# Performance work log

Measured on AMD Instinct MI355X. Metric: run time of the kernel, lower is better.

The kernel has to match this reference:

```python
import jax, jax.numpy as jnp
import numpy as np

B, S, D, H = 4, 1024, 256, 8  # batch, seq, d_model (== head_dim), n_heads
SCALE = 1.0 / float(np.sqrt(D))  # source references undefined self.scale; use 1/sqrt(d_model)


def setup_inputs() -> dict:
    key = jax.random.key(0)
    ks = jax.random.split(key, 11)
    w = 0.02
    return {
        "value_input": jax.random.normal(ks[0], (B, S, D), dtype=jnp.float32),
        "key_input": jax.random.normal(ks[1], (B, S, D), dtype=jnp.float32),
        "query_input": jax.random.normal(ks[2], (B, S, D), dtype=jnp.float32),
        "Wv": jax.random.normal(ks[3], (D, D * H), dtype=jnp.float32) * w,
        "bv": jnp.zeros((D * H,), dtype=jnp.float32),
        "Wk": jax.random.normal(ks[4], (D, D * H), dtype=jnp.float32) * w,
        "bk": jnp.zeros((D * H,), dtype=jnp.float32),
        "Wq": jax.random.normal(ks[5], (D, D * H), dtype=jnp.float32) * w,
        "bq": jnp.zeros((D * H,), dtype=jnp.float32),
        "Wo": jax.random.normal(ks[6], (D * H, D), dtype=jnp.float32) * w,
        "bo": jnp.zeros((D,), dtype=jnp.float32),
    }


def reference(value_input, key_input, query_input, Wv, bv, Wk, bk, Wq, bq, Wo, bo):
    # Fused QKV-style projections, then split into heads along last dim.
    # torch.split(..., d_model, dim=-1) == reshape to (B, S, H, D).
    v = (value_input @ Wv + bv).reshape(B, S, H, D)
    k = (key_input @ Wk + bk).reshape(B, S, H, D)
    q = (query_input @ Wq + bq).reshape(B, S, H, D)
    # Source: dot = k @ q^T  -> scores[b,h,key_pos,query_pos]
    scores = jnp.einsum('bkhd,bqhd->bhkq', k, q) * SCALE
    # Softmax over dim=-1 == the QUERY axis (faithful to source, nonstandard).
    attn = jax.nn.softmax(scores, axis=-1)
    # attn @ v : contract query axis with v's seq axis -> output indexed by key pos
    out_h = jnp.einsum('bhkq,bqhd->bkhd', attn, v)
    concat = out_h.reshape(B, S, H * D)
    return concat @ Wo + bo
```

## Files before the change

### kernel.cpp

```cpp
#include <hip/hip_runtime.h>
#include <cstddef>
#include <cstdint>

#define Bz 4
#define Sz 1024
#define Dm 256
#define Hh 8
#define DHh 2048
#define SCALE 0.0625f

typedef __attribute__((ext_vector_type(8))) short short8;
typedef __attribute__((ext_vector_type(16))) float f32x16;

__device__ inline unsigned short f2bf(float f){
  unsigned u = __float_as_uint(f);
  u += 0x7FFFu + ((u >> 16) & 1u);
  return (unsigned short)(u >> 16);
}
__device__ inline unsigned pk2(float a, float b){
  return (unsigned)f2bf(a) | ((unsigned)f2bf(b) << 16);
}
__device__ inline void gll16(const void* g, void* l){
  __builtin_amdgcn_global_load_lds((const __attribute__((address_space(1))) unsigned*)g,
                                   (__attribute__((address_space(3))) unsigned*)l, 16, 0, 0);
}
__device__ inline short8 lds8(const char* p){ return *(const short8*)p; }
__device__ inline f32x16 MM(short8 a, short8 b, f32x16 c){
  return __builtin_amdgcn_mfma_f32_32x32x16_bf16(a, b, c, 0, 0, 0);
}
__device__ inline f32x16 z16(){ f32x16 v;
#pragma unroll
  for(int i=0;i<16;i++) v[i]=0.f; return v; }

__global__ __launch_bounds__(256) void cvt_a(
    const float* __restrict__ S0, const float* __restrict__ S1, const float* __restrict__ S2,
    unsigned short* __restrict__ D0, unsigned short* __restrict__ D1, unsigned short* __restrict__ D2){
  const int bx = blockIdx.x;
  const int seg = bx >> 10;
  const float* src = seg==0 ? S0 : seg==1 ? S1 : S2;
  unsigned short* dst = seg==0 ? D0 : seg==1 ? D1 : D2;
  const int i = (bx & 1023)*256 + threadIdx.x;
  float4 v = ((const float4*)src)[i];
  ushort4 o; o.x=f2bf(v.x); o.y=f2bf(v.y); o.z=f2bf(v.z); o.w=f2bf(v.w);
  ((ushort4*)dst)[i] = o;
}

__global__ __launch_bounds__(256) void cvt_w(
    const float* __restrict__ W0, const float* __restrict__ W1,
    const float* __restrict__ W2, const float* __restrict__ W3,
    unsigned short* __restrict__ T0, unsigned short* __restrict__ T1,
    unsigned short* __restrict__ T2, unsigned short* __restrict__ T3){
  __shared__ float t[32][33];
  const int z = blockIdx.z;
  const float* W = z==0 ? W0 : z==1 ? W1 : z==2 ? W2 : W3;
  unsigned short* T = z==0 ? T0 : z==1 ? T1 : z==2 ? T2 : T3;
  const int K = (z<3) ? 256 : 2048;
  const int N = (z<3) ? 2048 : 256;
  const int n0 = (z<3) ? blockIdx.x*32 : blockIdx.y*32;
  const int k0 = (z<3) ? blockIdx.y*32 : blockIdx.x*32;
  const int a = threadIdx.x >> 5, c = threadIdx.x & 31;
#pragma unroll
  for(int p=0;p<4;p++)
    t[a + p*8][c] = W[(size_t)(k0 + a + p*8)*N + n0 + c];
  __syncthreads();
#pragma unroll
  for(int p=0;p<4;p++)
    T[(size_t)(n0 + a + p*8)*K + k0 + c] = f2bf(t[c][a + p*8]);
}

template<int VAR>
__global__ __launch_bounds__(256) void gemm_proj(const unsigned short* __restrict__ A,
    const unsigned short* __restrict__ Bt, const float* __restrict__ bias,
    unsigned short* __restrict__ C){
  __shared__ __align__(16) char sm[65536];
  const int tid = threadIdx.x, w = tid>>6, lane = tid&63, l31 = lane&31, hp = lane>>5;
  const int wm = (w>>1)*64, wn = (w&1)*64;
  const int bm = blockIdx.y*128, bn = blockIdx.x*128;
  f32x16 acc[2][2]; acc[0][0]=z16(); acc[0][1]=z16(); acc[1][0]=z16(); acc[1][1]=z16();

  auto STAGE = [&](int db, int kk){
#pragma unroll
    for(int j=0;j<4;j++){
      int ci = (w*4+j)*64 + lane;
      int m = ci>>3, sl = ci&7;
      gll16(A  + (size_t)(bm+m)*256 + kk + ((sl ^ (m&7))<<3), sm + db*32768 + (w*4+j)*1024);
      gll16(Bt + (size_t)(bn+m)*256 + kk + ((sl ^ (m&7))<<3), sm + db*32768 + 16384 + (w*4+j)*1024);
    }
  };

  STAGE(0, 0);
  __syncthreads();
  int db = 0;
  for(int t=0; t<4; ++t){
    if(t<3) STAGE(db^1, (t+1)*64);
    const char* base = sm + db*32768;
#pragma unroll
    for(int s=0;s<4;s++){
      int m0 = wm + l31, m1 = wm + 32 + l31;
      int n0 = wn + l31, n1 = wn + 32 + l31;
      short8 a0 = lds8(base + m0*128 + (((s*2+hp) ^ (m0&7))<<4));
      short8 a1 = lds8(base + m1*128 + (((s*2+hp) ^ (m1&7))<<4));
      short8 b0 = lds8(base + 16384 + n0*128 + (((s*2+hp) ^ (n0&7))<<4));
      short8 b1 = lds8(base + 16384 + n1*128 + (((s*2+hp) ^ (n1&7))<<4));
      acc[0][0] = MM(a0,b0,acc[0][0]); acc[0][1] = MM(a0,b1,acc[0][1]);
      acc[1][0] = MM(a1,b0,acc[1][0]); acc[1][1] = MM(a1,b1,acc[1][1]);
    }
    __syncthreads();
    db ^= 1;
  }
#pragma unroll
  for(int nh=0; nh<2; nh++){
    int ncol = bn + wn + nh*32 + l31;
    float bb = bias[ncol];
#pragma unroll
    for(int mh=0; mh<2; mh++){
      if(VAR == 2){
        int hidx = ncol >> 8, d = ncol & 255;
#pragma unroll
        for(int g=0; g<4; g++){
          int mrow = bm + wm + mh*32 + 8*g + 4*hp;
          int batch = mrow >> 10, sin = mrow & 1023;
          unsigned u0 = pk2(acc[mh][nh][4*g+0] + bb, acc[mh][nh][4*g+1] + bb);
          unsigned u1 = pk2(acc[mh][nh][4*g+2] + bb, acc[mh][nh][4*g+3] + bb);
          uint2 uu; uu.x = u0; uu.y = u1;
          *(uint2*)(C + ((size_t)((batch*Hh + hidx)*Dm + d))*Sz + sin) = uu;
        }
      } else {
#pragma unroll
        for(int r=0; r<16; r++){
          int mrow = bm + wm + mh*32 + (r&3) + 8*(r>>2) + 4*hp;
          float v = acc[mh][nh][r] + bb;
          if(VAR == 1) v *= SCALE;
          C[(size_t)mrow*DHh + ncol] = f2bf(v);
        }
      }
    }
  }
}

__global__ __launch_bounds__(512, 2) void attn_mfma(
    const unsigned short* __restrict__ Kp, const unsigned short* __restrict__ Qp,
    const unsigned short* __restrict__ Vt, unsigned short* __restrict__ Oc){
  __shared__ __align__(16) char sm[133120];
  const int tid = threadIdx.x, w = tid>>6, lane = tid&63, l31 = lane&31, hp = lane>>5;
  const int set = w>>2, ws = w&3;
  const int bid = blockIdx.x;
  const int g = (bid & 7)*4 + (bid >> 6);
  const int b = g >> 3, h = g & 7;
  const int brow0 = ((bid >> 3) & 7) * 128;
  const size_t vtbase = ((size_t)((b*Hh + h)*Dm))*Sz;

  short8 kp[16];
  {
    const unsigned short* kr = Kp + (size_t)(b*Sz + brow0 + ws*32 + l31)*DHh + h*Dm + hp*8;
#pragma unroll
    for(int ki=0; ki<16; ki++) kp[ki] = *(const short8*)(kr + ki*16);
  }
  f32x16 acc[8];
#pragma unroll
  for(int f=0; f<8; f++) acc[f] = z16();
  float m_run = -3.0e38f, l_run = 0.f;

  auto STAGE = [&](int db, int it){
    const int kv0 = set*512 + it*32;
    char* qpD = sm + db*65536 + set*16384;
    char* vtD = sm + db*65536 + 32768 + set*16384;
#pragma unroll
    for(int j=0; j<4; j++){
      int ci = (ws*4+j)*64 + lane;
      int c = ci>>5, sl5 = ci&31;
      gll16(Qp + (size_t)(b*Sz + kv0 + c)*DHh + h*Dm + ((sl5 ^ c)<<3),
            qpD + (ws*4+j)*1024);
      int dp = ci>>3, sv = (ci&7) ^ (dp&7);
      int d = dp*2 + (sv>>2), co = (sv&3)*8;
      gll16(Vt + vtbase + (size_t)d*Sz + kv0 + co, vtD + (ws*4+j)*1024);
    }
  };

  STAGE(0, 0);
  __syncthreads();
  int db = 0;
  for(int it=0; it<16; ++it){
    if(it<15) STAGE(db^1, it+1);
    const char* qpL = sm + db*65536 + set*16384;
    const char* vtL = sm + db*65536 + 32768 + set*16384;
    f32x16 S = z16();
#pragma unroll
    for(int ki=0; ki<16; ki++){
      short8 a = lds8(qpL + l31*512 + (((ki*2+hp) ^ l31)<<4));
      S = MM(a, kp[ki], S);
    }
    float tmax = S[0];
#pragma unroll
    for(int r=1; r<16; r++) tmax = fmaxf(tmax, S[r]);
    tmax = fmaxf(tmax, __shfl_xor(tmax, 32));
    if(!__all(tmax <= m_run + 8.0f)){
      float mnew = fmaxf(m_run, tmax);
      float alpha = __expf(m_run - mnew);
      m_run = mnew; l_run *= alpha;
#pragma unroll
      for(int r=0; r<16; r++){
        int rr = (r&3) + 8*(r>>2) + 4*hp;
        float ar = __shfl(alpha, rr);
#pragma unroll
        for(int f=0; f<8; f++) acc[f][r] *= ar;
      }
    }
    float lsum = 0.f;
#pragma unroll
    for(int r=0; r<16; r++){ S[r] = __expf(S[r] - m_run); lsum += S[r]; }
    lsum += __shfl_xor(lsum, 32);
    l_run += lsum;
    short8 pa[2];
#pragma unroll
    for(int t=0; t<2; t++){
      unsigned w01 = pk2(S[t*8+0], S[t*8+1]);
      unsigned w23 = pk2(S[t*8+2], S[t*8+3]);
      unsigned w45 = pk2(S[t*8+4], S[t*8+5]);
      unsigned w67 = pk2(S[t*8+6], S[t*8+7]);
      unsigned x01 = __shfl_xor(w01, 32), x23 = __shfl_xor(w23, 32);
      unsigned x45 = __shfl_xor(w45, 32), x67 = __shfl_xor(w67, 32);
      union { unsigned u[4]; short8 s8; } U;
      if(hp == 0){ U.u[0]=w01; U.u[1]=w23; U.u[2]=x01; U.u[3]=x23; }
      else       { U.u[0]=x45; U.u[1]=x67; U.u[2]=w45; U.u[3]=w67; }
      pa[t] = U.s8;
    }
#pragma unroll
    for(int t=0; t<2; t++){
#pragma unroll
      for(int f=0; f<8; f++){
        int d = f*32 + l31;
        int dp = d>>1;
        int slot = (d&1)*4 + t*2 + hp;
        short8 vfr = lds8(vtL + dp*128 + ((slot ^ (dp&7))<<4));
        acc[f] = MM(pa[t], vfr, acc[f]);
      }
    }
    __syncthreads();
    db ^= 1;
  }
  float* stats = (float*)(sm + 131072);
  if(lane < 32){ stats[(w*32 + lane)*2 + 0] = m_run; stats[(w*32 + lane)*2 + 1] = l_run; }
  __syncthreads();
  float* mg = (float*)sm + ws*8192;
  if(set == 1){
    float mA = stats[(ws*32 + l31)*2 + 0];
    float mf = fmaxf(mA, m_run);
    float bB = __expf(m_run - mf);
#pragma unroll
    for(int r=0; r<16; r++){
      int rr = (r&3) + 8*(r>>2) + 4*hp;
      float br = __shfl(bB, rr);
#pragma unroll
      for(int f=0; f<8; f++) mg[rr*256 + f*32 + l31] = acc[f][r]*br;
    }
  }
  __syncthreads();
  if(set == 0){
    float mB = stats[((4+ws)*32 + l31)*2 + 0];
    float lB = stats[((4+ws)*32 + l31)*2 + 1];
    float mf = fmaxf(m_run, mB);
    float bA = __expf(m_run - mf), bBv = __expf(mB - mf);
    float inv = 1.0f / (l_run*bA + lB*bBv);
#pragma unroll
    for(int r=0; r<16; r++){
      int rr = (r&3) + 8*(r>>2) + 4*hp;
      float bAr = __shfl(bA, rr);
      float invr = __shfl(inv, rr);
      int srow = brow0 + ws*32 + rr;
#pragma unroll
      for(int f=0; f<8; f++){
        float v = (acc[f][r]*bAr + mg[rr*256 + f*32 + l31]) * invr;
        Oc[(size_t)(b*Sz + srow)*DHh + h*Dm + f*32 + l31] = f2bf(v);
      }
    }
  }
}

__global__ __launch_bounds__(256) void gemm_out(const unsigned short* __restrict__ A,
    const unsigned short* __restrict__ Bt, const float* __restrict__ bias,
    float* __restrict__ C){
  __shared__ __align__(16) char sm[32768];
  const int tid = threadIdx.x, w = tid>>6, lane = tid&63, l31 = lane&31, hp = lane>>5;
  const int wm = (w>>1)*32, wn = (w&1)*32;
  const int bm = blockIdx.y*64, bn = blockIdx.x*64;
  f32x16 acc = z16();

  auto STAGE = [&](int db, int kk){
#pragma unroll
    for(int j=0; j<2; j++){
      int ci = (w*2+j)*64 + lane;
      int m = ci>>3, sl = ci&7;
      gll16(A  + (size_t)(bm+m)*DHh + kk + ((sl ^ (m&7))<<3), sm + db*16384 + (w*2+j)*1024);
      gll16(Bt + (size_t)(bn+m)*DHh + kk + ((sl ^ (m&7))<<3), sm + db*16384 + 8192 + (w*2+j)*1024);
    }
  };

  STAGE(0, 0);
  __syncthreads();
  int db = 0;
  for(int t=0; t<32; ++t){
    if(t<31) STAGE(db^1, (t+1)*64);
    const char* base = sm + db*16384;
#pragma unroll
    for(int s=0; s<4; s++){
      int m0 = wm + l31, n0 = wn + l31;
      short8 a = lds8(base + m0*128 + (((s*2+hp) ^ (m0&7))<<4));
      short8 b = lds8(base + 8192 + n0*128 + (((s*2+hp) ^ (n0&7))<<4));
      acc = MM(a, b, acc);
    }
    __syncthreads();
    db ^= 1;
  }
  float bb = bias[bn + wn + l31];
#pragma unroll
  for(int r=0; r<16; r++){
    int mrow = bm + wm + (r&3) + 8*(r>>2) + 4*hp;
    C[(size_t)mrow*Dm + bn + wn + l31] = acc[r] + bb;
  }
}

extern "C" void kernel_launch(void* const* d_in, const int* in_sizes, int n_in,
                              void* d_out, int out_size, void* d_ws, size_t ws_size,
                              hipStream_t stream){
  (void)in_sizes; (void)n_in; (void)out_size; (void)ws_size;
  const float* value_in = (const float*)d_in[0];
  const float* key_in   = (const float*)d_in[1];
  const float* query_in = (const float*)d_in[2];
  const float* Wv = (const float*)d_in[3];
  const float* bv = (const float*)d_in[4];
  const float* Wk = (const float*)d_in[5];
  const float* bk = (const float*)d_in[6];
  const float* Wq = (const float*)d_in[7];
  const float* bq = (const float*)d_in[8];
  const float* Wo = (const float*)d_in[9];
  const float* bo = (const float*)d_in[10];

  char* ws = (char*)d_ws;
  unsigned short* av  = (unsigned short*)(ws + ((size_t) 0u<<20));
  unsigned short* ak  = (unsigned short*)(ws + ((size_t) 2u<<20));
  unsigned short* aq  = (unsigned short*)(ws + ((size_t) 4u<<20));
  unsigned short* wtv = (unsigned short*)(ws + ((size_t) 6u<<20));
  unsigned short* wtk = (unsigned short*)(ws + ((size_t) 7u<<20));
  unsigned short* wtq = (unsigned short*)(ws + ((size_t) 8u<<20));
  unsigned short* wto = (unsigned short*)(ws + ((size_t) 9u<<20));
  unsigned short* vt  = (unsigned short*)(ws + ((size_t)10u<<20));
  unsigned short* kb  = (unsigned short*)(ws + ((size_t)26u<<20));
  unsigned short* qb  = (unsigned short*)(ws + ((size_t)42u<<20));
  unsigned short* cc  = (unsigned short*)(ws + ((size_t)58u<<20));

  cvt_a<<<3072, 256, 0, stream>>>(value_in, key_in, query_in, av, ak, aq);
  cvt_w<<<dim3(64, 8, 4), 256, 0, stream>>>(Wv, Wk, Wq, Wo, wtv, wtk, wtq, wto);

  gemm_proj<2><<<dim3(16, 32), 256, 0, stream>>>(av, wtv, bv, vt);
  gemm_proj<1><<<dim3(16, 32), 256, 0, stream>>>(ak, wtk, bk, kb);
  gemm_proj<0><<<dim3(16, 32), 256, 0, stream>>>(aq, wtq, bq, qb);

  attn_mfma<<<256, 512, 0, stream>>>(kb, qb, vt, cc);

  gemm_out<<<dim3(4, 64), 256, 0, stream>>>(cc, wto, bo, (float*)d_out);
}
```

Before: 208.2 us.

## Merge conversion and projection launches; shrink attention blocks and drop double buffering

Folds the two fp32-to-bf16 conversion kernels into one launch and the three projection GEMMs into a single z-indexed launch, removing launch gaps and letting the projections share the GPU concurrently. The attention kernel is reshaped from 512-thread, 128-row blocks with double-buffered LDS to 256-thread, 64-row blocks with a single LDS buffer. That halves shared memory per block and doubles the grid, aiming for more resident blocks. The cost is that loads are no longer overlapped with compute, since each tile is staged between two barriers.

```diff
diff --git a/kernel.cpp b/kernel.cpp
--- a/kernel.cpp
+++ b/kernel.cpp
@@ -32,32 +32,33 @@
 #pragma unroll
   for(int i=0;i<16;i++) v[i]=0.f; return v; }
 
-__global__ __launch_bounds__(256) void cvt_a(
+__global__ __launch_bounds__(256) void cvt_all(
     const float* __restrict__ S0, const float* __restrict__ S1, const float* __restrict__ S2,
-    unsigned short* __restrict__ D0, unsigned short* __restrict__ D1, unsigned short* __restrict__ D2){
-  const int bx = blockIdx.x;
-  const int seg = bx >> 10;
-  const float* src = seg==0 ? S0 : seg==1 ? S1 : S2;
-  unsigned short* dst = seg==0 ? D0 : seg==1 ? D1 : D2;
-  const int i = (bx & 1023)*256 + threadIdx.x;
-  float4 v = ((const float4*)src)[i];
-  ushort4 o; o.x=f2bf(v.x); o.y=f2bf(v.y); o.z=f2bf(v.z); o.w=f2bf(v.w);
-  ((ushort4*)dst)[i] = o;
-}
-
-__global__ __launch_bounds__(256) void cvt_w(
+    unsigned short* __restrict__ D0, unsigned short* __restrict__ D1, unsigned short* __restrict__ D2,
     const float* __restrict__ W0, const float* __restrict__ W1,
     const float* __restrict__ W2, const float* __restrict__ W3,
     unsigned short* __restrict__ T0, unsigned short* __restrict__ T1,
     unsigned short* __restrict__ T2, unsigned short* __restrict__ T3){
   __shared__ float t[32][33];
-  const int z = blockIdx.z;
+  int bx = blockIdx.x;
+  if(bx < 3072){
+    const int seg = bx >> 10;
+    const float* src = seg==0 ? S0 : seg==1 ? S1 : S2;
+    unsigned short* dst = seg==0 ? D0 : seg==1 ? D1 : D2;
+    const int i = (bx & 1023)*256 + threadIdx.x;
+    float4 v = ((const float4*)src)[i];
+    ushort4 o; o.x=f2bf(v.x); o.y=f2bf(v.y); o.z=f2bf(v.z); o.w=f2bf(v.w);
+    ((ushort4*)dst)[i] = o;
+    return;
+  }
+  bx -= 3072;
+  const int z = bx >> 9, inner = bx & 511;
   const float* W = z==0 ? W0 : z==1 ? W1 : z==2 ? W2 : W3;
   unsigned short* T = z==0 ? T0 : z==1 ? T1 : z==2 ? T2 : T3;
   const int K = (z<3) ? 256 : 2048;
   const int N = (z<3) ? 2048 : 256;
-  const int n0 = (z<3) ? blockIdx.x*32 : blockIdx.y*32;
-  const int k0 = (z<3) ? blockIdx.y*32 : blockIdx.x*32;
+  const int n0 = (z<3) ? (inner & 63)*32 : (inner & 7)*32;
+  const int k0 = (z<3) ? (inner >> 6)*32 : (inner >> 3)*32;
   const int a = threadIdx.x >> 5, c = threadIdx.x & 31;
 #pragma unroll
   for(int p=0;p<4;p++)
@@ -68,11 +69,21 @@
     T[(size_t)(n0 + a + p*8)*K + k0 + c] = f2bf(t[c][a + p*8]);
 }
 
-template<int VAR>
-__global__ __launch_bounds__(256) void gemm_proj(const unsigned short* __restrict__ A,
-    const unsigned short* __restrict__ Bt, const float* __restrict__ bias,
-    unsigned short* __restrict__ C){
+__global__ __launch_bounds__(256) void gemm_proj_all(
+    const unsigned short* __restrict__ A0, const unsigned short* __restrict__ A1,
+    const unsigned short* __restrict__ A2,
+    const unsigned short* __restrict__ B0, const unsigned short* __restrict__ B1,
+    const unsigned short* __restrict__ B2,
+    const float* __restrict__ bias0, const float* __restrict__ bias1,
+    const float* __restrict__ bias2,
+    unsigned short* __restrict__ C0, unsigned short* __restrict__ C1,
+    unsigned short* __restrict__ C2){
   __shared__ __align__(16) char sm[65536];
+  const int z = blockIdx.z;
+  const unsigned short* A = z==0 ? A0 : z==1 ? A1 : A2;
+  const unsigned short* Bt = z==0 ? B0 : z==1 ? B1 : B2;
+  const float* bias = z==0 ? bias0 : z==1 ? bias1 : bias2;
+  unsigned short* C = z==0 ? C0 : z==1 ? C1 : C2;
   const int tid = threadIdx.x, w = tid>>6, lane = tid&63, l31 = lane&31, hp = lane>>5;
   const int wm = (w>>1)*64, wn = (w&1)*64;
   const int bm = blockIdx.y*128, bn = blockIdx.x*128;
@@ -114,45 +125,45 @@
     float bb = bias[ncol];
 #pragma unroll
     for(int mh=0; mh<2; mh++){
-      if(VAR == 2){
+      if(z == 0){
         int hidx = ncol >> 8, d = ncol & 255;
 #pragma unroll
-        for(int g=0; g<4; g++){
-          int mrow = bm + wm + mh*32 + 8*g + 4*hp;
+        for(int gq=0; gq<4; gq++){
+          int mrow = bm + wm + mh*32 + 8*gq + 4*hp;
           int batch = mrow >> 10, sin = mrow & 1023;
-          unsigned u0 = pk2(acc[mh][nh][4*g+0] + bb, acc[mh][nh][4*g+1] + bb);
-          unsigned u1 = pk2(acc[mh][nh][4*g+2] + bb, acc[mh][nh][4*g+3] + bb);
+          unsigned u0 = pk2(acc[mh][nh][4*gq+0] + bb, acc[mh][nh][4*gq+1] + bb);
+          unsigned u1 = pk2(acc[mh][nh][4*gq+2] + bb, acc[mh][nh][4*gq+3] + bb);
           uint2 uu; uu.x = u0; uu.y = u1;
           *(uint2*)(C + ((size_t)((batch*Hh + hidx)*Dm + d))*Sz + sin) = uu;
         }
       } else {
+        float sc = (z == 1) ? SCALE : 1.0f;
 #pragma unroll
         for(int r=0; r<16; r++){
           int mrow = bm + wm + mh*32 + (r&3) + 8*(r>>2) + 4*hp;
-          float v = acc[mh][nh][r] + bb;
-          if(VAR == 1) v *= SCALE;
-          C[(size_t)mrow*DHh + ncol] = f2bf(v);
+          C[(size_t)mrow*DHh + ncol] = f2bf((acc[mh][nh][r] + bb) * sc);
         }
       }
     }
   }
 }
 
-__global__ __launch_bounds__(512, 2) void attn_mfma(
+__global__ __launch_bounds__(256, 2) void attn_mfma(
     const unsigned short* __restrict__ Kp, const unsigned short* __restrict__ Qp,
     const unsigned short* __restrict__ Vt, unsigned short* __restrict__ Oc){
-  __shared__ __align__(16) char sm[133120];
+  __shared__ __align__(16) char sm[66560];
   const int tid = threadIdx.x, w = tid>>6, lane = tid&63, l31 = lane&31, hp = lane>>5;
-  const int set = w>>2, ws = w&3;
+  const int rg = w&1, set = w>>1;
   const int bid = blockIdx.x;
-  const int g = (bid & 7)*4 + (bid >> 6);
-  const int b = g >> 3, h = g & 7;
-  const int brow0 = ((bid >> 3) & 7) * 128;
+  const int xcd = bid & 7, inner = bid >> 3;
+  const int rb = inner & 15, gsub = inner >> 4;
+  const int g = gsub*8 + xcd, b = g >> 3, h = g & 7;
+  const int brow0 = rb * 64;
   const size_t vtbase = ((size_t)((b*Hh + h)*Dm))*Sz;
 
   short8 kp[16];
   {
-    const unsigned short* kr = Kp + (size_t)(b*Sz + brow0 + ws*32 + l31)*DHh + h*Dm + hp*8;
+    const unsigned short* kr = Kp + (size_t)(b*Sz + brow0 + rg*32 + l31)*DHh + h*Dm + hp*8;
 #pragma unroll
     for(int ki=0; ki<16; ki++) kp[ki] = *(const short8*)(kr + ki*16);
   }
@@ -160,30 +171,27 @@
 #pragma unroll
   for(int f=0; f<8; f++) acc[f] = z16();
   float m_run = -3.0e38f, l_run = 0.f;
-
-  auto STAGE = [&](int db, int it){
+  char* qpL = sm + set*16384;
+  char* vtL = sm + 32768 + set*16384;
+
+  auto STAGE = [&](int it){
     const int kv0 = set*512 + it*32;
-    char* qpD = sm + db*65536 + set*16384;
-    char* vtD = sm + db*65536 + 32768 + set*16384;
-#pragma unroll
-    for(int j=0; j<4; j++){
-      int ci = (ws*4+j)*64 + lane;
+#pragma unroll
+    for(int j=0; j<8; j++){
+      int slot = j*2 + rg;
+      int ci = slot*64 + lane;
       int c = ci>>5, sl5 = ci&31;
       gll16(Qp + (size_t)(b*Sz + kv0 + c)*DHh + h*Dm + ((sl5 ^ c)<<3),
-            qpD + (ws*4+j)*1024);
+            qpL + slot*1024);
       int dp = ci>>3, sv = (ci&7) ^ (dp&7);
       int d = dp*2 + (sv>>2), co = (sv&3)*8;
-      gll16(Vt + vtbase + (size_t)d*Sz + kv0 + co, vtD + (ws*4+j)*1024);
+      gll16(Vt + vtbase + (size_t)d*Sz + kv0 + co, vtL + slot*1024);
     }
   };
 
-  STAGE(0, 0);
-  __syncthreads();
-  int db = 0;
+  STAGE(0);
+  __syncthreads();
   for(int it=0; it<16; ++it){
-    if(it<15) STAGE(db^1, it+1);
-    const char* qpL = sm + db*65536 + set*16384;
-    const char* vtL = sm + db*65536 + 32768 + set*16384;
     f32x16 S = z16();
 #pragma unroll
     for(int ki=0; ki<16; ki++){
@@ -236,15 +244,19 @@
         acc[f] = MM(pa[t], vfr, acc[f]);
       }
     }
-    __syncthreads();
-    db ^= 1;
-  }
-  float* stats = (float*)(sm + 131072);
+    if(it < 15){
+      __syncthreads();
+      STAGE(it+1);
+      __syncthreads();
+    }
+  }
+  __syncthreads();
+  float* stats = (float*)(sm + 65536);
   if(lane < 32){ stats[(w*32 + lane)*2 + 0] = m_run; stats[(w*32 + lane)*2 + 1] = l_run; }
   __syncthreads();
-  float* mg = (float*)sm + ws*8192;
+  float* mg = (float*)sm + rg*8192;
   if(set == 1){
-    float mA = stats[(ws*32 + l31)*2 + 0];
+    float mA = stats[(rg*32 + l31)*2 + 0];
     float mf = fmaxf(mA, m_run);
     float bB = __expf(m_run - mf);
 #pragma unroll
@@ -257,8 +269,8 @@
   }
   __syncthreads();
   if(set == 0){
-    float mB = stats[((4+ws)*32 + l31)*2 + 0];
-    float lB = stats[((4+ws)*32 + l31)*2 + 1];
+    float mB = stats[((2+rg)*32 + l31)*2 + 0];
+    float lB = stats[((2+rg)*32 + l31)*2 + 1];
     float mf = fmaxf(m_run, mB);
     float bA = __expf(m_run - mf), bBv = __expf(mB - mf);
     float inv = 1.0f / (l_run*bA + lB*bBv);
@@ -267,7 +279,7 @@
       int rr = (r&3) + 8*(r>>2) + 4*hp;
       float bAr = __shfl(bA, rr);
       float invr = __shfl(inv, rr);
-      int srow = brow0 + ws*32 + rr;
+      int srow = brow0 + rg*32 + rr;
 #pragma unroll
       for(int f=0; f<8; f++){
         float v = (acc[f][r]*bAr + mg[rr*256 + f*32 + l31]) * invr;
@@ -349,14 +361,13 @@
   unsigned short* qb  = (unsigned short*)(ws + ((size_t)42u<<20));
   unsigned short* cc  = (unsigned short*)(ws + ((size_t)58u<<20));
 
-  cvt_a<<<3072, 256, 0, stream>>>(value_in, key_in, query_in, av, ak, aq);
-  cvt_w<<<dim3(64, 8, 4), 256, 0, stream>>>(Wv, Wk, Wq, Wo, wtv, wtk, wtq, wto);
-
-  gemm_proj<2><<<dim3(16, 32), 256, 0, stream>>>(av, wtv, bv, vt);
-  gemm_proj<1><<<dim3(16, 32), 256, 0, stream>>>(ak, wtk, bk, kb);
-  gemm_proj<0><<<dim3(16, 32), 256, 0, stream>>>(aq, wtq, bq, qb);
-
-  attn_mfma<<<256, 512, 0, stream>>>(kb, qb, vt, cc);
+  cvt_all<<<5120, 256, 0, stream>>>(value_in, key_in, query_in, av, ak, aq,
+                                    Wv, Wk, Wq, Wo, wtv, wtk, wtq, wto);
+
+  gemm_proj_all<<<dim3(16, 32, 3), 256, 0, stream>>>(
+      av, ak, aq, wtv, wtk, wtq, bv, bk, bq, vt, kb, qb);
+
+  attn_mfma<<<512, 256, 0, stream>>>(kb, qb, vt, cc);
 
   gemm_out<<<dim3(4, 64), 256, 0, stream>>>(cc, wto, bo, (float*)d_out);
 }
```

New measurement: 253.3 us. +21.7%, slower.
